# Performance work log

Hardware: AMD Instinct MI355X
Metric: run time of the kernel (lower is better)

## Reference

```python
import jax, jax.numpy as jnp
import numpy as np


def setup_inputs() -> dict:
    key = jax.random.key(0)
    k1, k2 = jax.random.split(key)
    N = 8192
    similarity = jax.random.normal(k1, (N, N), dtype=jnp.float32)
    text_to_img_mapping = jax.random.randint(k2, (N,), 0, N, dtype=jnp.int64)
    return {"similarity": similarity, "text_to_img_mapping": text_to_img_mapping}


def reference(similarity, text_to_img_mapping):
    n_text, n_img = similarity.shape
    rows = jnp.arange(n_text)
    # text->image CE: mean over text rows of -log_softmax(sim, axis=1)[i, map[i]]
    lsm_rows = jax.nn.log_softmax(similarity, axis=1)
    text_loss = -jnp.mean(lsm_rows[rows, text_to_img_mapping])
    # image->text CE with multi-hot soft targets mask[img, txt] = 1 iff map[txt] == img.
    # -sum(mask * log_softmax(sim.T, axis=1)) / n_img
    #   == -sum_i log_softmax(sim, axis=0)[i, map[i]] / n_img  (gather, no NxN mask)
    lsm_cols = jax.nn.log_softmax(similarity, axis=0)
    visual_loss = -jnp.sum(lsm_cols[rows, text_to_img_mapping]) / n_img
    return (text_loss + visual_loss) / 2.0
```

## Files before the change

kernel.cpp:

```cpp
#include <hip/hip_runtime.h>
#include <hip/hip_bf16.h>
#include <math.h>

#define N 8192
#define RB 32
#define T1 512
#define NRC (N / RB)
#define CPT 16

typedef float v4f __attribute__((ext_vector_type(4)));


__device__ __forceinline__ unsigned short f2bf(float f) {
    unsigned int u = __float_as_uint(f);
    return (unsigned short)((u + 0x7fffu + ((u >> 16) & 1u)) >> 16);
}
__device__ __forceinline__ float bf2f(unsigned short h) {
    return __uint_as_float((unsigned int)h << 16);
}

__global__ __launch_bounds__(T1)
void stage1(const float* __restrict__ sim, const long long* __restrict__ map,
            unsigned short* __restrict__ colSb,
            float* __restrict__ blkPart) {
    const int tid = threadIdx.x;
    const int rc = blockIdx.x;
    const int rowBase = rc * RB;

    float cs[CPT];
    #pragma unroll
    for (int k = 0; k < CPT; ++k) cs[k] = 0.f;

    __shared__ float lrow[RB][T1];
    __shared__ float rowLog[RB];

    float gsum = 0.f;

    #pragma unroll 4
    for (int r = 0; r < RB; ++r) {
        const int row = rowBase + r;
        const v4f* p = (const v4f*)(sim + (size_t)row * N);
        v4f v0 = __builtin_nontemporal_load(p + tid);
        v4f v1 = __builtin_nontemporal_load(p + tid + T1);
        v4f v2 = __builtin_nontemporal_load(p + tid + 2 * T1);
        v4f v3 = __builtin_nontemporal_load(p + tid + 3 * T1);

        if (tid == 0) {
            int c = (int)map[row];
            gsum += sim[(size_t)row * N + c];
        }

        float e0 = __expf(v0.x), e1 = __expf(v0.y), e2 = __expf(v0.z), e3 = __expf(v0.w);
        float e4 = __expf(v1.x), e5 = __expf(v1.y), e6 = __expf(v1.z), e7 = __expf(v1.w);
        float e8 = __expf(v2.x), e9 = __expf(v2.y), eA = __expf(v2.z), eB = __expf(v2.w);
        float eC = __expf(v3.x), eD = __expf(v3.y), eE = __expf(v3.z), eF = __expf(v3.w);

        cs[0] += e0; cs[1] += e1; cs[2]  += e2; cs[3]  += e3;
        cs[4] += e4; cs[5] += e5; cs[6]  += e6; cs[7]  += e7;
        cs[8] += e8; cs[9] += e9; cs[10] += eA; cs[11] += eB;
        cs[12] += eC; cs[13] += eD; cs[14] += eE; cs[15] += eF;

        float rp = (((e0 + e1) + (e2 + e3)) + ((e4 + e5) + (e6 + e7)))
                 + (((e8 + e9) + (eA + eB)) + ((eC + eD) + (eE + eF)));
        lrow[r][tid] = rp;
    }
    __syncthreads();

    {
        const int r = tid >> 4, j = tid & 15;
        float s = 0.f;
        #pragma unroll
        for (int k = 0; k < T1 / 16; ++k)
            s += lrow[r][j + 16 * k];
        s += __shfl_xor(s, 1);
        s += __shfl_xor(s, 2);
        s += __shfl_xor(s, 4);
        s += __shfl_xor(s, 8);
        if (j == 0) rowLog[r] = __logf(s);
    }
    __syncthreads();

    if (tid == 0) {
        float b = -2.0f * gsum;
        #pragma unroll
        for (int r = 0; r < RB; ++r) b += rowLog[r];
        blkPart[rc] = b;
    }

    unsigned short* rowp = colSb + (size_t)rc * N;
    #pragma unroll
    for (int k = 0; k < 4; ++k) {
        uint2 w;
        w.x = (unsigned int)f2bf(cs[4 * k + 0]) | ((unsigned int)f2bf(cs[4 * k + 1]) << 16);
        w.y = (unsigned int)f2bf(cs[4 * k + 2]) | ((unsigned int)f2bf(cs[4 * k + 3]) << 16);
        *(uint2*)(rowp + 4 * tid + 2048 * k) = w;
    }
}

__global__ __launch_bounds__(512)
void stage2(const unsigned short* __restrict__ colSb,
            const long long* __restrict__ map,
            float* __restrict__ colDot) {
    const int tid = threadIdx.x;
    const int cl = tid & 31;
    const int slice = tid >> 5;
    const int g = blockIdx.x * 32 + cl;

    __shared__ int cnt[32];
    if (tid < 32) cnt[tid] = 0;
    __syncthreads();

    #pragma unroll 4
    for (int k = 0; k < N / 512; ++k) {
        int c = (int)map[k * 512 + tid];
        if ((c >> 5) == blockIdx.x) atomicAdd(&cnt[c & 31], 1);
    }

    float s = 0.f;
    #pragma unroll 4
    for (int k = 0; k < NRC / 16; ++k)
        s += bf2f(__builtin_nontemporal_load(
                 colSb + (size_t)(slice * (NRC / 16) + k) * N + g));

    __shared__ float lds[16][32];
    lds[slice][cl] = s;
    __syncthreads();

    if (tid < 32) {
        float t = 0.f;
        #pragma unroll
        for (int w = 0; w < 16; ++w) t += lds[w][tid];
        float v = (float)cnt[tid] * __logf(t);
        v += __shfl_xor(v, 1);
        v += __shfl_xor(v, 2);
        v += __shfl_xor(v, 4);
        v += __shfl_xor(v, 8);
        v += __shfl_xor(v, 16);
        if (tid == 0) colDot[blockIdx.x] = v;
    }
}

__global__ __launch_bounds__(256)
void stage3(const float* __restrict__ blkPart, const float* __restrict__ colDot,
            float* __restrict__ out) {
    const int tid = threadIdx.x;
    float v = blkPart[tid] + colDot[tid];
    #pragma unroll
    for (int off = 32; off >= 1; off >>= 1)
        v += __shfl_xor(v, off);
    __shared__ float red[4];
    const int wave = tid >> 6, lane = tid & 63;
    if (lane == 0) red[wave] = v;
    __syncthreads();
    if (tid == 0)
        out[0] = (red[0] + red[1] + red[2] + red[3]) / (2.0f * (float)N);
}

extern "C" void kernel_launch(void* const* d_in, const int* in_sizes, int n_in,
                              void* d_out, int out_size, void* d_ws, size_t ws_size,
                              hipStream_t stream) {
    const float* sim = (const float*)d_in[0];
    const long long* map = (const long long*)d_in[1];
    float* out = (float*)d_out;

    char* ws = (char*)d_ws;
    unsigned short* colSb = (unsigned short*)ws;
    float* blkPart = (float*)(ws + (size_t)NRC * N * 2);
    float* colDot  = blkPart + NRC;

    stage1<<<NRC, T1, 0, stream>>>(sim, map, colSb, blkPart);
    stage2<<<N / 32, 512, 0, stream>>>(colSb, map, colDot);
    stage3<<<1, 256, 0, stream>>>(blkPart, colDot, out);
}
```

Baseline: 53.13 us.

## Split stage1 rows across two column halves for more blocks

Stage1 now uses a 2D grid where each block handles 32 rows over half the columns with 256 threads, doubling the block count from 256 to 512. Partial row exp-sums are written to global memory and combined plus logged in stage2, and the gather term is counted only by the half that owns the target column. The aim is better occupancy and load spread across CUs on the bandwidth-bound pass, at the cost of an extra small global round-trip and more work in stage2 and stage3.

Measured after the change: 52.55 us. No clear change (-1.1%).

```diff
diff --git a/kernel.cpp b/kernel.cpp
--- a/kernel.cpp
+++ b/kernel.cpp
@@ -4,9 +4,9 @@
 
 #define N 8192
 #define RB 32
-#define T1 512
+#define CB 4096
+#define T1 256
 #define NRC (N / RB)
-#define CPT 16
 
 typedef float v4f __attribute__((ext_vector_type(4)));
 
@@ -22,24 +22,26 @@
 __global__ __launch_bounds__(T1)
 void stage1(const float* __restrict__ sim, const long long* __restrict__ map,
             unsigned short* __restrict__ colSb,
-            float* __restrict__ blkPart) {
+            float* __restrict__ rowP,
+            float* __restrict__ gPart) {
     const int tid = threadIdx.x;
-    const int rc = blockIdx.x;
+    const int h  = blockIdx.x;
+    const int rc = blockIdx.y;
     const int rowBase = rc * RB;
+    const int colBase = h * CB;
 
-    float cs[CPT];
+    float cs[16];
     #pragma unroll
-    for (int k = 0; k < CPT; ++k) cs[k] = 0.f;
+    for (int k = 0; k < 16; ++k) cs[k] = 0.f;
 
     __shared__ float lrow[RB][T1];
-    __shared__ float rowLog[RB];
 
     float gsum = 0.f;
 
-    #pragma unroll 4
+    #pragma unroll 2
     for (int r = 0; r < RB; ++r) {
         const int row = rowBase + r;
-        const v4f* p = (const v4f*)(sim + (size_t)row * N);
+        const v4f* p = (const v4f*)(sim + (size_t)row * N + colBase);
         v4f v0 = __builtin_nontemporal_load(p + tid);
         v4f v1 = __builtin_nontemporal_load(p + tid + T1);
         v4f v2 = __builtin_nontemporal_load(p + tid + 2 * T1);
@@ -47,7 +49,8 @@
 
         if (tid == 0) {
             int c = (int)map[row];
-            gsum += sim[(size_t)row * N + c];
+            if ((c >> 12) == h)
+                gsum += sim[(size_t)row * N + c];
         }
 
         float e0 = __expf(v0.x), e1 = __expf(v0.y), e2 = __expf(v0.z), e3 = __expf(v0.w);
@@ -67,40 +70,34 @@
     __syncthreads();
 
     {
-        const int r = tid >> 4, j = tid & 15;
+        const int r = tid >> 3, j = tid & 7;
         float s = 0.f;
         #pragma unroll
-        for (int k = 0; k < T1 / 16; ++k)
-            s += lrow[r][j + 16 * k];
+        for (int k = 0; k < T1 / 8; ++k)
+            s += lrow[r][j + 8 * k];
         s += __shfl_xor(s, 1);
         s += __shfl_xor(s, 2);
         s += __shfl_xor(s, 4);
-        s += __shfl_xor(s, 8);
-        if (j == 0) rowLog[r] = __logf(s);
-    }
-    __syncthreads();
-
-    if (tid == 0) {
-        float b = -2.0f * gsum;
-        #pragma unroll
-        for (int r = 0; r < RB; ++r) b += rowLog[r];
-        blkPart[rc] = b;
+        if (j == 0) rowP[(size_t)h * N + rowBase + r] = s;
     }
 
-    unsigned short* rowp = colSb + (size_t)rc * N;
+    if (tid == 0) gPart[rc * 2 + h] = -2.0f * gsum;
+
+    unsigned short* rowp = colSb + (size_t)rc * N + colBase;
     #pragma unroll
     for (int k = 0; k < 4; ++k) {
         uint2 w;
         w.x = (unsigned int)f2bf(cs[4 * k + 0]) | ((unsigned int)f2bf(cs[4 * k + 1]) << 16);
         w.y = (unsigned int)f2bf(cs[4 * k + 2]) | ((unsigned int)f2bf(cs[4 * k + 3]) << 16);
-        *(uint2*)(rowp + 4 * tid + 2048 * k) = w;
+        *(uint2*)(rowp + 4 * tid + (CB / 4) * k) = w;
     }
 }
 
 __global__ __launch_bounds__(512)
 void stage2(const unsigned short* __restrict__ colSb,
             const long long* __restrict__ map,
-            float* __restrict__ colDot) {
+            const float* __restrict__ rowP,
+            float* __restrict__ colDot, float* __restrict__ rowDot) {
     const int tid = threadIdx.x;
     const int cl = tid & 31;
     const int slice = tid >> 5;
@@ -137,23 +134,37 @@
         v += __shfl_xor(v, 8);
         v += __shfl_xor(v, 16);
         if (tid == 0) colDot[blockIdx.x] = v;
+    } else if (tid >= 64 && tid < 96) {
+        const int r = blockIdx.x * 32 + (tid - 64);
+        float v = __logf(rowP[r] + rowP[N + r]);
+        v += __shfl_xor(v, 1);
+        v += __shfl_xor(v, 2);
+        v += __shfl_xor(v, 4);
+        v += __shfl_xor(v, 8);
+        v += __shfl_xor(v, 16);
+        if (tid == 64) rowDot[blockIdx.x] = v;
     }
 }
 
-__global__ __launch_bounds__(256)
-void stage3(const float* __restrict__ blkPart, const float* __restrict__ colDot,
-            float* __restrict__ out) {
+__global__ __launch_bounds__(512)
+void stage3(const float* __restrict__ colDot, const float* __restrict__ rowDot,
+            const float* __restrict__ gPart, float* __restrict__ out) {
     const int tid = threadIdx.x;
-    float v = blkPart[tid] + colDot[tid];
+    float v = gPart[tid];
+    if (tid < NRC) v += colDot[tid] + rowDot[tid];
     #pragma unroll
     for (int off = 32; off >= 1; off >>= 1)
         v += __shfl_xor(v, off);
-    __shared__ float red[4];
+    __shared__ float red[8];
     const int wave = tid >> 6, lane = tid & 63;
     if (lane == 0) red[wave] = v;
     __syncthreads();
-    if (tid == 0)
-        out[0] = (red[0] + red[1] + red[2] + red[3]) / (2.0f * (float)N);
+    if (tid == 0) {
+        float t = 0.f;
+        #pragma unroll
+        for (int w = 0; w < 8; ++w) t += red[w];
+        out[0] = t / (2.0f * (float)N);
+    }
 }
 
 extern "C" void kernel_launch(void* const* d_in, const int* in_sizes, int n_in,
@@ -165,10 +176,13 @@
 
     char* ws = (char*)d_ws;
     unsigned short* colSb = (unsigned short*)ws;
-    float* blkPart = (float*)(ws + (size_t)NRC * N * 2);
-    float* colDot  = blkPart + NRC;
+    float* rowP   = (float*)(ws + (size_t)NRC * N * 2);
+    float* gPart  = rowP + 2 * N;
+    float* colDot = gPart + 2 * NRC;
+    float* rowDot = colDot + NRC;
 
-    stage1<<<NRC, T1, 0, stream>>>(sim, map, colSb, blkPart);
-    stage2<<<N / 32, 512, 0, stream>>>(colSb, map, colDot);
-    stage3<<<1, 256, 0, stream>>>(blkPart, colDot, out);
+    dim3 g1(2, NRC);
+    stage1<<<g1, T1, 0, stream>>>(sim, map, colSb, rowP, gPart);
+    stage2<<<N / 32, 512, 0, stream>>>(colSb, map, rowP, colDot, rowDot);
+    stage3<<<1, 512, 0, stream>>>(colDot, rowDot, gPart, out);
 }
```
